# Kernel tuning notes

Measured on AMD Instinct MI355X. Metric: run time of the kernel, lower is better.

The kernel has to match this reference:

```python
import jax, jax.numpy as jnp
import numpy as np

TEMPERATURE = 0.07
TOP_MARGIN = 0.95
BOTTOM_MARGIN = 0.05

BATCH = 8192
DIM = 1024


def setup_inputs() -> dict:
    key = jax.random.key(0)
    kA, kB = jax.random.split(key)
    embedding_A = jax.random.normal(kA, (BATCH, DIM), dtype=jnp.float32)
    embedding_B = jax.random.normal(kB, (BATCH, DIM), dtype=jnp.float32)
    return {"embedding_A": embedding_A, "embedding_B": embedding_B}


def _l2norm(x):
    return x * jax.lax.rsqrt(jnp.sum(x * x, axis=-1, keepdims=True))


def reference(embedding_A, embedding_B):
    a = _l2norm(embedding_A)
    b = _l2norm(embedding_B)
    B = a.shape[0]
    sim = a @ b.T                                   # [B, B]
    pos = jnp.diagonal(sim)                         # [B]
    eye = jnp.eye(B, dtype=bool)
    upper = pos[:, None] * TOP_MARGIN
    lower = pos[:, None] * BOTTOM_MARGIN
    neg_mask = (sim <= upper) & (sim >= lower) & ~eye   # [B, B]

    # Per-row CE over [positive, hard negatives] == masked logsumexp - pos/tau.
    z = sim / TEMPERATURE
    full_mask = neg_mask | eye                      # positive always included
    masked = jnp.where(full_mask, z, -jnp.inf)
    m = jnp.max(masked, axis=1, keepdims=True)      # finite: diag always present
    lse = m[:, 0] + jnp.log(jnp.sum(jnp.exp(masked - m), axis=1))
    per_row = lse - pos / TEMPERATURE               # [B]

    valid = jnp.any(neg_mask, axis=1)               # rows with >=1 negative
    count = jnp.sum(valid)
    total = jnp.sum(jnp.where(valid, per_row, 0.0))
    return total / jnp.maximum(count, 1).astype(total.dtype)
```

## Files before the change

kernel.cpp:

```cpp
#include <hip/hip_runtime.h>
#include <hip/hip_bf16.h>

#define BATCH 8192
#define DIM   1024
#define INV_TAU (1.0f / 0.07f)
#define TOPM 0.95f
#define BOTM 0.05f

#define BM 256
#define BN 256
#define BK 64
#define NT (DIM / BK)

typedef __attribute__((ext_vector_type(4))) float f32x4;
typedef __attribute__((ext_vector_type(8))) short bf16x8;

typedef __attribute__((address_space(3))) void       lds_void_t;
typedef const __attribute__((address_space(1))) void gbl_void_t;

__device__ inline void async_copy16(const void* g, void* l) {
    __builtin_amdgcn_global_load_lds((gbl_void_t*)g, (lds_void_t*)l, 16, 0, 0);
}

__device__ inline unsigned short f2bf(float f) {
    __hip_bfloat16 h = __float2bfloat16(f);
    return *reinterpret_cast<unsigned short*>(&h);
}

__global__ __launch_bounds__(256) void prep_kernel(
    const float* __restrict__ A, const float* __restrict__ B,
    unsigned short* __restrict__ An, unsigned short* __restrict__ Bn,
    float* __restrict__ pos, float* __restrict__ S)
{
    int row = blockIdx.x;
    int t = threadIdx.x;
    const float4* a4 = (const float4*)(A + (size_t)row * DIM);
    const float4* b4 = (const float4*)(B + (size_t)row * DIM);
    float4 av = a4[t];
    float4 bv = b4[t];
    float sa = av.x*av.x + av.y*av.y + av.z*av.z + av.w*av.w;
    float sb = bv.x*bv.x + bv.y*bv.y + bv.z*bv.z + bv.w*bv.w;
    float dp = av.x*bv.x + av.y*bv.y + av.z*bv.z + av.w*bv.w;
    #pragma unroll
    for (int d = 32; d > 0; d >>= 1) {
        sa += __shfl_down(sa, d);
        sb += __shfl_down(sb, d);
        dp += __shfl_down(dp, d);
    }
    __shared__ float red[3][4];
    int lane = t & 63, w = t >> 6;
    if (lane == 0) { red[0][w] = sa; red[1][w] = sb; red[2][w] = dp; }
    __syncthreads();
    sa = red[0][0] + red[0][1] + red[0][2] + red[0][3];
    sb = red[1][0] + red[1][1] + red[1][2] + red[1][3];
    dp = red[2][0] + red[2][1] + red[2][2] + red[2][3];
    float ra = rsqrtf(sa);
    float rb = rsqrtf(sb);
    if (t == 0) {
        pos[row] = dp * ra * rb;
        S[row] = 0.0f;
    }
    ushort4 oa, ob;
    oa.x = f2bf(av.x * ra); oa.y = f2bf(av.y * ra);
    oa.z = f2bf(av.z * ra); oa.w = f2bf(av.w * ra);
    ob.x = f2bf(bv.x * rb); ob.y = f2bf(bv.y * rb);
    ob.z = f2bf(bv.z * rb); ob.w = f2bf(bv.w * rb);
    ((ushort4*)(An + (size_t)row * DIM))[t] = oa;
    ((ushort4*)(Bn + (size_t)row * DIM))[t] = ob;
}

__global__ __launch_bounds__(512, 2) void sim_loss_kernel(
    const unsigned short* __restrict__ An, const unsigned short* __restrict__ Bn,
    const float* __restrict__ pos, float* __restrict__ S)
{
    __shared__ char lds[131072];

    int tid  = threadIdx.x;
    int lane = tid & 63;
    int wave = tid >> 6;
    int wm = wave >> 2, wn = wave & 3;
    int fr = lane & 15;
    int q  = lane >> 4;

    int bid = blockIdx.x;

#define BASES(g, rB, cB) do {                                                        \
    int xcd_ = bid & 7, jj_ = bid >> 3;                                              \
    int qr_ = (g) >> 1, qc_ = ((g) & 1) ^ (qr_ & 1);                                 \
    (rB) = (qr_ * 16 + (xcd_ >> 1) * 4 + (jj_ >> 3)) * BM;                           \
    (cB) = (qc_ * 16 + (xcd_ & 1) * 8 + (jj_ & 7)) * BN;                             \
} while (0)

    f32x4 acc[8][4] = {};
    bf16x8 a[4][2];
    bf16x8 b0[2][2];
    bf16x8 b1[2][2];

    int sw = (fr & 7) << 4;
    int c0 = (q * 16) ^ sw;
    int c1 = (64 + q * 16) ^ sw;
    int aRow = (wm * 128 + fr) * 128;
    int bRow = (wn * 64 + fr) * 128;

    int strow = tid >> 3;
    int scb   = ((tid & 7) * 16) ^ ((strow & 7) << 4);
    int ldst = tid * 16;

#define PANELS(rB, cB, pA, pB) do {                                                  \
    (pA) = (const char*)An + (size_t)((rB) + strow) * 2048 + scb;                    \
    (pB) = (const char*)Bn + (size_t)((cB) + strow) * 2048 + scb;                    \
} while (0)

#define STAGE(gbase, u, h, ldsdst) do {                                              \
    async_copy16((gbase) + (size_t)(h) * 262144 + (size_t)(u) * 128,                 \
                 (ldsdst) + (h) * 16384 + ldst);                                     \
    async_copy16((gbase) + (size_t)(h) * 262144 + 131072 + (size_t)(u) * 128,        \
                 (ldsdst) + (h) * 16384 + 8192 + ldst);                              \
} while (0)

#define LDA_(p, mh) do {                                                             \
    const char* _s = lds + (p) * 32768;                                              \
    _Pragma("unroll") for (int m = 0; m < 4; ++m) {                                  \
        a[m][0] = *(const bf16x8*)(_s + aRow + (mh) * 8192 + m * 2048 + c0);         \
        a[m][1] = *(const bf16x8*)(_s + aRow + (mh) * 8192 + m * 2048 + c1);         \
    }                                                                                \
} while (0)

#define LDB_(arr, p, nh) do {                                                        \
    const char* _s = lds + 65536 + (p) * 32768;                                      \
    _Pragma("unroll") for (int n = 0; n < 2; ++n) {                                  \
        arr[n][0] = *(const bf16x8*)(_s + bRow + (nh) * 4096 + n * 2048 + c0);       \
        arr[n][1] = *(const bf16x8*)(_s + bRow + (nh) * 4096 + n * 2048 + c1);       \
    }                                                                                \
} while (0)

#define MM_(barr, mo, no) do {                                                       \
    _Pragma("unroll") for (int m = 0; m < 4; ++m)                                    \
    _Pragma("unroll") for (int n = 0; n < 2; ++n) {                                  \
        acc[(mo)+m][(no)+n] = __builtin_amdgcn_mfma_f32_16x16x32_bf16(               \
            a[m][0], barr[n][0], acc[(mo)+m][(no)+n], 0, 0, 0);                      \
        acc[(mo)+m][(no)+n] = __builtin_amdgcn_mfma_f32_16x16x32_bf16(               \
            a[m][1], barr[n][1], acc[(mo)+m][(no)+n], 0, 0, 0);                      \
    }                                                                                \
} while (0)

#define BAR() __builtin_amdgcn_s_barrier()
#define SCH() __builtin_amdgcn_sched_barrier(0)
#define LGKM(n) do { asm volatile("s_waitcnt lgkmcnt(" #n ")" ::: "memory");         \
                     SCH(); } while (0)
#define VMC(n)  asm volatile("s_waitcnt vmcnt(" #n ")" ::: "memory")
#define PRI1() __builtin_amdgcn_s_setprio(1)
#define PRI0() __builtin_amdgcn_s_setprio(0)

#define KTILE(p, pA_, uA, pB_, uB) do {                                              \
    char* stA = lds + ((p) ^ 1) * 32768;                                             \
    char* stB = lds + 65536 + ((p) ^ 1) * 32768;                                     \
                                                             \
    LDA_((p), 0); LDB_(b0, (p), 0); STAGE((pB_), (uB), 0, stB);                      \
    LGKM(8); BAR();                                                                  \
    LGKM(0); PRI1(); MM_(b0, 0, 0); PRI0(); BAR();                                   \
                                                             \
    LDB_(b1, (p), 1); STAGE((pB_), (uB), 1, stB);                                    \
    BAR();                                                                           \
    LGKM(0); PRI1(); MM_(b1, 0, 2); PRI0(); VMC(4); BAR();                           \
                                                             \
    LDA_((p), 1); STAGE((pA_), (uA), 0, stA);                                        \
    BAR();                                                                           \
    LGKM(0); PRI1(); MM_(b1, 4, 2); PRI0(); BAR();                                   \
                                                             \
    STAGE((pA_), (uA), 1, stA);                                                      \
    BAR();                                                                           \
    PRI1(); MM_(b0, 4, 0); PRI0(); VMC(2); BAR();                                    \
} while (0)

    int rowB, colB;
    BASES(0, rowB, colB);
    const char *gAc, *gBc;
    PANELS(rowB, colB, gAc, gBc);

    STAGE(gAc, 0, 0, lds);
    STAGE(gAc, 0, 1, lds);
    STAGE(gBc, 0, 0, lds + 65536);
    STAGE(gBc, 0, 1, lds + 65536);
    VMC(0);
    BAR();

    #pragma unroll 1
    for (int g = 0; g < 4; ++g) {
        int gn = (g < 3) ? g + 1 : 3;
        int rowBn, colBn;
        BASES(gn, rowBn, colBn);
        const char *gAn2, *gBn2;
        PANELS(rowBn, colBn, gAn2, gBn2);

        #pragma unroll 1
        for (int tt = 0; tt < 7; ++tt) {
            KTILE(0, gAc, 2 * tt + 1, gBc, 2 * tt + 1);
            KTILE(1, gAc, 2 * tt + 2, gBc, 2 * tt + 2);
        }
        KTILE(0, gAc, 15, gBc, 15);
        KTILE(1, gAn2, 0, gBn2, 0);

        #pragma unroll
        for (int m = 0; m < 8; ++m) {
            #pragma unroll
            for (int j2 = 0; j2 < 4; ++j2) {
                int i = rowB + wm * 128 + m * 16 + q * 4 + j2;
                float p  = pos[i];
                float up = TOPM * p, lo = BOTM * p;
                float rs = 0.0f;
                #pragma unroll
                for (int n = 0; n < 4; ++n) {
                    float sv = acc[m][n][j2];
                    int col = colB + wn * 64 + n * 16 + fr;
                    if (sv <= up && sv >= lo && col != i)
                        rs += __expf((sv - p) * INV_TAU);
                }
                #pragma unroll
                for (int d = 1; d < 16; d <<= 1)
                    rs += __shfl_xor(rs, d);
                if (fr == 0 && rs != 0.0f)
                    atomicAdd(&S[i], rs);
            }
        }
        #pragma unroll
        for (int m2 = 0; m2 < 8; ++m2)
            #pragma unroll
            for (int n2 = 0; n2 < 4; ++n2)
                acc[m2][n2] = (f32x4){0.0f, 0.0f, 0.0f, 0.0f};

        gAc = gAn2; gBc = gBn2; rowB = rowBn; colB = colBn;
    }
    VMC(0);

#undef BASES
#undef PANELS
#undef STAGE
#undef LDA_
#undef LDB_
#undef MM_
#undef BAR
#undef SCH
#undef LGKM
#undef VMC
#undef PRI1
#undef PRI0
#undef KTILE
}

__global__ __launch_bounds__(256) void finalize_kernel(
    const float* __restrict__ S, float* __restrict__ out)
{
    int t = threadIdx.x;
    float tot = 0.0f;
    int c = 0;
    for (int i = t; i < BATCH; i += 256) {
        float s = S[i];
        if (s > 0.0f) { tot += log1pf(s); c += 1; }
    }
    #pragma unroll
    for (int d = 32; d > 0; d >>= 1) {
        tot += __shfl_down(tot, d);
        c   += __shfl_down(c, d);
    }
    __shared__ float st[4];
    __shared__ int   sc[4];
    int lane = t & 63, w = t >> 6;
    if (lane == 0) { st[w] = tot; sc[w] = c; }
    __syncthreads();
    if (t == 0) {
        float T = st[0] + st[1] + st[2] + st[3];
        int   C = sc[0] + sc[1] + sc[2] + sc[3];
        out[0] = T / (float)(C > 0 ? C : 1);
    }
}

extern "C" void kernel_launch(void* const* d_in, const int* in_sizes, int n_in,
                              void* d_out, int out_size, void* d_ws, size_t ws_size,
                              hipStream_t stream) {
    const float* A = (const float*)d_in[0];
    const float* B = (const float*)d_in[1];

    char* ws = (char*)d_ws;
    unsigned short* An = (unsigned short*)ws;
    unsigned short* Bn = An + (size_t)BATCH * DIM;
    float* pos = (float*)(Bn + (size_t)BATCH * DIM);
    float* S   = pos + BATCH;
    float* out = (float*)d_out;

    prep_kernel<<<BATCH, 256, 0, stream>>>(A, B, An, Bn, pos, S);
    sim_loss_kernel<<<256, 512, 0, stream>>>(An, Bn, pos, S);
    finalize_kernel<<<1, 256, 0, stream>>>(S, out);
}
```

Measured before the change: 210.7 us.

## Restructure K-tile pipeline into two phases with B prefetched two tiles ahead

```diff
diff --git a/kernel.cpp b/kernel.cpp
--- a/kernel.cpp
+++ b/kernel.cpp
@@ -146,31 +146,26 @@
 
 #define BAR() __builtin_amdgcn_s_barrier()
 #define SCH() __builtin_amdgcn_sched_barrier(0)
-#define LGKM(n) do { asm volatile("s_waitcnt lgkmcnt(" #n ")" ::: "memory");         \
-                     SCH(); } while (0)
+#define LGKM0() asm volatile("s_waitcnt lgkmcnt(0)" ::: "memory")
 #define VMC(n)  asm volatile("s_waitcnt vmcnt(" #n ")" ::: "memory")
 #define PRI1() __builtin_amdgcn_s_setprio(1)
 #define PRI0() __builtin_amdgcn_s_setprio(0)
 
 #define KTILE(p, pA_, uA, pB_, uB) do {                                              \
     char* stA = lds + ((p) ^ 1) * 32768;                                             \
-    char* stB = lds + 65536 + ((p) ^ 1) * 32768;                                     \
-                                                             \
-    LDA_((p), 0); LDB_(b0, (p), 0); STAGE((pB_), (uB), 0, stB);                      \
-    LGKM(8); BAR();                                                                  \
-    LGKM(0); PRI1(); MM_(b0, 0, 0); PRI0(); BAR();                                   \
-                                                             \
-    LDB_(b1, (p), 1); STAGE((pB_), (uB), 1, stB);                                    \
-    BAR();                                                                           \
-    LGKM(0); PRI1(); MM_(b1, 0, 2); PRI0(); VMC(4); BAR();                           \
-                                                             \
-    LDA_((p), 1); STAGE((pA_), (uA), 0, stA);                                        \
-    BAR();                                                                           \
-    LGKM(0); PRI1(); MM_(b1, 4, 2); PRI0(); BAR();                                   \
-                                                             \
-    STAGE((pA_), (uA), 1, stA);                                                      \
-    BAR();                                                                           \
-    PRI1(); MM_(b0, 4, 0); PRI0(); VMC(2); BAR();                                    \
+    char* stB = lds + 65536 + (p) * 32768;                                           \
+                                                 \
+    BAR(); SCH();                                                                    \
+    LDA_((p), 0); LDB_(b0, (p), 0); LDB_(b1, (p), 1);                                \
+    STAGE((pA_), (uA), 0, stA); STAGE((pA_), (uA), 1, stA);                          \
+    PRI1(); MM_(b0, 0, 0); MM_(b1, 0, 2); PRI0();                                    \
+    LGKM0();                                                                         \
+                                                 \
+    BAR(); SCH();                                                                    \
+    LDA_((p), 1);                                                                    \
+    STAGE((pB_), (uB), 0, stB); STAGE((pB_), (uB), 1, stB);                          \
+    PRI1(); MM_(b1, 4, 2); MM_(b0, 4, 0); PRI0();                                    \
+    LGKM0(); VMC(4);                                                                 \
 } while (0)
 
     int rowB, colB;
@@ -182,8 +177,9 @@
     STAGE(gAc, 0, 1, lds);
     STAGE(gBc, 0, 0, lds + 65536);
     STAGE(gBc, 0, 1, lds + 65536);
-    VMC(0);
-    BAR();
+    STAGE(gBc, 1, 0, lds + 98304);
+    STAGE(gBc, 1, 1, lds + 98304);
+    VMC(4);
 
     #pragma unroll 1
     for (int g = 0; g < 4; ++g) {
@@ -195,11 +191,11 @@
 
         #pragma unroll 1
         for (int tt = 0; tt < 7; ++tt) {
-            KTILE(0, gAc, 2 * tt + 1, gBc, 2 * tt + 1);
-            KTILE(1, gAc, 2 * tt + 2, gBc, 2 * tt + 2);
+            KTILE(0, gAc, 2 * tt + 1, gBc, 2 * tt + 2);
+            KTILE(1, gAc, 2 * tt + 2, gBc, 2 * tt + 3);
         }
-        KTILE(0, gAc, 15, gBc, 15);
-        KTILE(1, gAn2, 0, gBn2, 0);
+        KTILE(0, gAc, 15, gBn2, 0);
+        KTILE(1, gAn2, 0, gBn2, 1);
 
         #pragma unroll
         for (int m = 0; m < 8; ++m) {
@@ -231,6 +227,7 @@
 
         gAc = gAn2; gBc = gBn2; rowB = rowBn; colB = colBn;
     }
+    LGKM0();
     VMC(0);
 
 #undef BASES
@@ -241,7 +238,7 @@
 #undef MM_
 #undef BAR
 #undef SCH
-#undef LGKM
+#undef LGKM0
 #undef VMC
 #undef PRI1
 #undef PRI0
```

Result: faster. 201.7 us (-4.3%).
